# Performance work log

Measured on AMD Instinct MI355X. Metric: run time of the kernel, lower is better.

## Reference

```python
import jax, jax.numpy as jnp
import numpy as np


def _gcn_conv(x, edge_index, W, b):
    """Standard PyG GCNConv: add self-loops, symmetric normalization, x@W, scatter-add, +bias."""
    n = x.shape[0]
    loop = jnp.arange(n, dtype=edge_index.dtype)
    src = jnp.concatenate([edge_index[0], loop])  # [E+N]
    dst = jnp.concatenate([edge_index[1], loop])  # [E+N]
    # degree of destination nodes (unit edge weights + self loops)
    deg = jax.ops.segment_sum(jnp.ones_like(dst, dtype=x.dtype), dst, num_segments=n)
    dinv = jnp.where(deg > 0, jax.lax.rsqrt(deg), 0.0)
    norm = dinv[src] * dinv[dst]  # [E+N]
    h = x @ W  # [N, C_out] -- transform before aggregation (fewer bytes moved)
    msg = h[src] * norm[:, None]  # gather + scale
    out = jax.ops.segment_sum(msg, dst, num_segments=n)  # scatter-add
    return out + b


def setup_inputs() -> dict:
    key = jax.random.key(0)
    k1, k2, k3, k4 = jax.random.split(key, 4)
    N, E, C_in, C_hid, C_out = 50000, 800000, 64, 64, 40
    x = jax.random.normal(k1, (N, C_in), dtype=jnp.float32)
    edge_index = jax.random.randint(k2, (2, E), 0, N, dtype=jnp.int64)
    # Glorot-ish init for weights, zeros for biases (PyG GCNConv default)
    W1 = jax.random.normal(k3, (C_in, C_hid), dtype=jnp.float32) * (1.0 / np.sqrt(C_in))
    b1 = jnp.zeros((C_hid,), dtype=jnp.float32)
    W2 = jax.random.normal(k4, (C_hid, C_out), dtype=jnp.float32) * (1.0 / np.sqrt(C_hid))
    b2 = jnp.zeros((C_out,), dtype=jnp.float32)
    return {"x": x, "edge_index": edge_index, "W1": W1, "b1": b1, "W2": W2, "b2": b2}


def reference(x, edge_index, W1, b1, W2, b2):
    h = jax.nn.relu(_gcn_conv(x, edge_index, W1, b1))
    # F.dropout(training=False) is identity in eval mode
    h = _gcn_conv(h, edge_index, W2, b2)
    return jax.nn.log_softmax(h, axis=1)
```

## Files before the change

### kernel.cpp

```cpp
#include <hip/hip_runtime.h>
#include <hip/hip_fp16.h>
#include <math.h>


#define SHIFT   8
#define RPB     256
#define NBMAX   256
#define SLACK   8192
#define CHUNK_P 2048

typedef float v2f __attribute__((ext_vector_type(2)));

__global__ void k_part_gemm(const int* __restrict__ ei32,
                            int* __restrict__ bcur,
                            unsigned int* __restrict__ ebkt, int E, int nb,
                            int npart,
                            const float* __restrict__ x,
                            const float* __restrict__ W1,
                            unsigned char* __restrict__ hs8, int n) {
    __shared__ __align__(16) float smem[2 * 64 * 68];
    if ((int)blockIdx.x < npart) {
        int* cnt   = (int*)smem;
        int* rbase = cnt + 256;
        int* is64p = rbase + 256;
        int* stash = is64p + 1;
        int t = threadIdx.x;
        cnt[t] = 0;
        if (t == 0) {
            int is64 = 1;
            for (int i = 0; i < 64; ++i)
                if (ei32[2 * i + 1] != 0) { is64 = 0; break; }
            *is64p = is64;
        }
        __syncthreads();
        int is64 = *is64p;
        int lo = blockIdx.x * CHUNK_P;
        int hi = lo + CHUNK_P; if (hi > E) hi = E;
        for (int e = lo + t; e < hi; e += 256) {
            int s, d;
            if (is64) { s = ei32[2 * e]; d = ei32[2 * (E + e)]; }
            else      { s = ei32[e];     d = ei32[E + e]; }
            stash[e - lo] = (int)(((unsigned int)d << 16) | (unsigned int)s);
            atomicAdd(&cnt[d >> SHIFT], 1);
        }
        __syncthreads();
        {
            int c = cnt[t];
            rbase[t] = c ? atomicAdd(&bcur[t], c) : 0;
            cnt[t] = 0;
        }
        __syncthreads();
        for (int e = lo + t; e < hi; e += 256) {
            unsigned int v = (unsigned int)stash[e - lo];
            int b = (int)(v >> 16) >> SHIFT;
            int pos = rbase[b] + atomicAdd(&cnt[b], 1);
            ebkt[pos] = (((v >> 16) & (RPB - 1)) << 16) | (v & 0xffffu);
        }
    } else {
        float* Wl = smem;
        float* Xl = smem + 64 * 68;
        int t  = threadIdx.x;
        int tr = t >> 4, tc = t & 15;
        int base = (blockIdx.x - npart) * 64;

        for (int i = t; i < 64 * 17; i += 256) {
            int k = i / 17, c4 = (i % 17) * 4;
            float4 w = make_float4(0.f, 0.f, 0.f, 0.f);
            if (c4 < 64) w = *(const float4*)&W1[k * 64 + c4];
            *(float4*)&Wl[k * 68 + c4] = w;
        }
        for (int rr = tr; rr < 64; rr += 16) {
            int row = base + rr; if (row >= n) row = n - 1;
            float4 v = *(const float4*)&x[(size_t)row * 64 + tc * 4];
            Xl[(tc * 4 + 0) * 68 + rr] = v.x;
            Xl[(tc * 4 + 1) * 68 + rr] = v.y;
            Xl[(tc * 4 + 2) * 68 + rr] = v.z;
            Xl[(tc * 4 + 3) * 68 + rr] = v.w;
        }
        __syncthreads();

        float acc[4][4] = {{0.f}};
#pragma unroll 8
        for (int k = 0; k < 64; ++k) {
            float4 xv = *(const float4*)&Xl[k * 68 + tr * 4];
            float4 wv = *(const float4*)&Wl[k * 68 + tc * 4];
            acc[0][0] = fmaf(xv.x, wv.x, acc[0][0]);
            acc[0][1] = fmaf(xv.x, wv.y, acc[0][1]);
            acc[0][2] = fmaf(xv.x, wv.z, acc[0][2]);
            acc[0][3] = fmaf(xv.x, wv.w, acc[0][3]);
            acc[1][0] = fmaf(xv.y, wv.x, acc[1][0]);
            acc[1][1] = fmaf(xv.y, wv.y, acc[1][1]);
            acc[1][2] = fmaf(xv.y, wv.z, acc[1][2]);
            acc[1][3] = fmaf(xv.y, wv.w, acc[1][3]);
            acc[2][0] = fmaf(xv.z, wv.x, acc[2][0]);
            acc[2][1] = fmaf(xv.z, wv.y, acc[2][1]);
            acc[2][2] = fmaf(xv.z, wv.z, acc[2][2]);
            acc[2][3] = fmaf(xv.z, wv.w, acc[2][3]);
            acc[3][0] = fmaf(xv.w, wv.x, acc[3][0]);
            acc[3][1] = fmaf(xv.w, wv.y, acc[3][1]);
            acc[3][2] = fmaf(xv.w, wv.z, acc[3][2]);
            acc[3][3] = fmaf(xv.w, wv.w, acc[3][3]);
        }
#pragma unroll
        for (int i = 0; i < 4; ++i) {
            int r = base + tr * 4 + i;
            if (r >= n) break;
            unsigned int w;
            w = (unsigned int)__builtin_amdgcn_cvt_pk_fp8_f32(
                    acc[i][0], acc[i][1], 0, false);
            w = (unsigned int)__builtin_amdgcn_cvt_pk_fp8_f32(
                    acc[i][2], acc[i][3], (int)w, true);
            ((unsigned int*)(hs8 + ((size_t)r << 6)))[tc] = w;
        }
    }
}

__global__ void k_build(const unsigned int* __restrict__ ebkt,
                        const int* __restrict__ bcur,
                        int* __restrict__ row_beg, int* __restrict__ row_end,
                        float* __restrict__ dinv,
                        unsigned short* __restrict__ csr_src, int N) {
    __shared__ int cnt[RPB];
    __shared__ int ssum[RPB];
    int t = threadIdx.x, b = blockIdx.x;
    int rows0 = b << SHIFT;
    cnt[t] = 0;
    __syncthreads();
    int lo = b * SLACK, hi = bcur[b];
    for (int e = lo + t; e < hi; e += 256)
        atomicAdd(&cnt[ebkt[e] >> 16], 1);
    __syncthreads();
    int c = cnt[t];
    ssum[t] = c;
    __syncthreads();
    for (int off = 1; off < 256; off <<= 1) {
        int u = (t >= off) ? ssum[t - off] : 0;
        __syncthreads();
        ssum[t] += u;
        __syncthreads();
    }
    int beg = lo + ssum[t] - c;
    int row = rows0 + t;
    if (row < N) {
        row_beg[row] = beg; row_end[row] = beg + c;
        dinv[row] = rsqrtf((float)c + 1.0f);
    }
    cnt[t] = beg;
    __syncthreads();
    for (int e = lo + t; e < hi; e += 256) {
        unsigned int v = ebkt[e];
        int pos = atomicAdd(&cnt[v >> 16], 1);
        csr_src[pos] = (unsigned short)(v & 0xffffu);
    }
}

__global__ void k_gather_relu64(const unsigned char* __restrict__ hs8,
                                const int* __restrict__ rbg,
                                const int* __restrict__ ren,
                                const unsigned short* __restrict__ ci,
                                const float* __restrict__ dinv,
                                const float* __restrict__ bias,
                                __half* __restrict__ out, int n) {
    int row = blockIdx.x * 4 + (threadIdx.x >> 6);
    if (row >= n) return;
    int lane = threadIdx.x & 63;
    int g = lane >> 3, q = lane & 7;
    int beg = rbg[row], end = ren[row];

    float dv = dinv[row];
    uint2 su = ((const uint2*)(hs8 + ((size_t)row << 6)))[q];

    float4 aa = make_float4(0.f, 0.f, 0.f, 0.f);
    float4 ab = make_float4(0.f, 0.f, 0.f, 0.f);
    for (int base = beg; base < end; base += 64) {
        int mm = end - base; if (mm > 64) mm = 64;
        int idx = (lane < mm) ? (int)ci[base + lane] : 0;
        for (int j = 0; 8 * j < mm; ++j) {
            int e = 8 * j + g;
            int s = __shfl(idx, e, 64);
            if (base + e < end) {
                float ds = dinv[s];
                uint2 u = ((const uint2*)(hs8 + ((size_t)s << 6)))[q];
                v2f f0 = __builtin_amdgcn_cvt_pk_f32_fp8((int)u.x, false);
                v2f f1 = __builtin_amdgcn_cvt_pk_f32_fp8((int)u.x, true);
                v2f f2 = __builtin_amdgcn_cvt_pk_f32_fp8((int)u.y, false);
                v2f f3 = __builtin_amdgcn_cvt_pk_f32_fp8((int)u.y, true);
                aa.x = fmaf(f0.x, ds, aa.x); aa.y = fmaf(f0.y, ds, aa.y);
                aa.z = fmaf(f1.x, ds, aa.z); aa.w = fmaf(f1.y, ds, aa.w);
                ab.x = fmaf(f2.x, ds, ab.x); ab.y = fmaf(f2.y, ds, ab.y);
                ab.z = fmaf(f3.x, ds, ab.z); ab.w = fmaf(f3.y, ds, ab.w);
            }
        }
    }
#pragma unroll
    for (int o = 8; o < 64; o <<= 1) {
        aa.x += __shfl_xor(aa.x, o, 64); aa.y += __shfl_xor(aa.y, o, 64);
        aa.z += __shfl_xor(aa.z, o, 64); aa.w += __shfl_xor(aa.w, o, 64);
        ab.x += __shfl_xor(ab.x, o, 64); ab.y += __shfl_xor(ab.y, o, 64);
        ab.z += __shfl_xor(ab.z, o, 64); ab.w += __shfl_xor(ab.w, o, 64);
    }
    v2f s0 = __builtin_amdgcn_cvt_pk_f32_fp8((int)su.x, false);
    v2f s1 = __builtin_amdgcn_cvt_pk_f32_fp8((int)su.x, true);
    v2f s2 = __builtin_amdgcn_cvt_pk_f32_fp8((int)su.y, false);
    v2f s3 = __builtin_amdgcn_cvt_pk_f32_fp8((int)su.y, true);
    float4 bv0 = *(const float4*)&bias[q * 8];
    float4 bv1 = *(const float4*)&bias[q * 8 + 4];
    float v0 = fmaxf((aa.x + s0.x * dv) * dv + bv0.x, 0.f);
    float v1 = fmaxf((aa.y + s0.y * dv) * dv + bv0.y, 0.f);
    float v2 = fmaxf((aa.z + s1.x * dv) * dv + bv0.z, 0.f);
    float v3 = fmaxf((aa.w + s1.y * dv) * dv + bv0.w, 0.f);
    float v4 = fmaxf((ab.x + s2.x * dv) * dv + bv1.x, 0.f);
    float v5 = fmaxf((ab.y + s2.y * dv) * dv + bv1.y, 0.f);
    float v6 = fmaxf((ab.z + s3.x * dv) * dv + bv1.z, 0.f);
    float v7 = fmaxf((ab.w + s3.y * dv) * dv + bv1.w, 0.f);
    if (lane < 8) {
        uint4 st;
        ((__half2*)&st)[0] = __floats2half2_rn(v0, v1);
        ((__half2*)&st)[1] = __floats2half2_rn(v2, v3);
        ((__half2*)&st)[2] = __floats2half2_rn(v4, v5);
        ((__half2*)&st)[3] = __floats2half2_rn(v6, v7);
        ((uint4*)(out + ((size_t)row << 6)))[q] = st;
    }
}

template<int COUT>
__global__ void k_gemm(const __half* __restrict__ xin,
                       const float* __restrict__ W,
                       const float* __restrict__ dinv,
                       __half* __restrict__ hs, int n) {
    __shared__ float Wl[64 * 68];
    __shared__ float Xl[64 * 68];
    int t  = threadIdx.x;
    int tr = t >> 4, tc = t & 15;
    int base = blockIdx.x * 64;

    for (int i = t; i < 64 * 17; i += 256) {
        int k = i / 17, c4 = (i % 17) * 4;
        float4 w = make_float4(0.f, 0.f, 0.f, 0.f);
        if (c4 < COUT) w = *(const float4*)&W[k * COUT + c4];
        *(float4*)&Wl[k * 68 + c4] = w;
    }
    for (int rr = tr; rr < 64; rr += 16) {
        int row = base + rr; if (row >= n) row = n - 1;
        uint2 u = *(const uint2*)&xin[(size_t)row * 64 + tc * 4];
        float2 a = __half22float2(*(__half2*)&u.x);
        float2 c = __half22float2(*(__half2*)&u.y);
        Xl[(tc * 4 + 0) * 68 + rr] = a.x;
        Xl[(tc * 4 + 1) * 68 + rr] = a.y;
        Xl[(tc * 4 + 2) * 68 + rr] = c.x;
        Xl[(tc * 4 + 3) * 68 + rr] = c.y;
    }
    __syncthreads();

    float acc[4][4] = {{0.f}};
#pragma unroll 8
    for (int k = 0; k < 64; ++k) {
        float4 xv = *(const float4*)&Xl[k * 68 + tr * 4];
        float4 wv = *(const float4*)&Wl[k * 68 + tc * 4];
        acc[0][0] = fmaf(xv.x, wv.x, acc[0][0]);
        acc[0][1] = fmaf(xv.x, wv.y, acc[0][1]);
        acc[0][2] = fmaf(xv.x, wv.z, acc[0][2]);
        acc[0][3] = fmaf(xv.x, wv.w, acc[0][3]);
        acc[1][0] = fmaf(xv.y, wv.x, acc[1][0]);
        acc[1][1] = fmaf(xv.y, wv.y, acc[1][1]);
        acc[1][2] = fmaf(xv.y, wv.z, acc[1][2]);
        acc[1][3] = fmaf(xv.y, wv.w, acc[1][3]);
        acc[2][0] = fmaf(xv.z, wv.x, acc[2][0]);
        acc[2][1] = fmaf(xv.z, wv.y, acc[2][1]);
        acc[2][2] = fmaf(xv.z, wv.z, acc[2][2]);
        acc[2][3] = fmaf(xv.z, wv.w, acc[2][3]);
        acc[3][0] = fmaf(xv.w, wv.x, acc[3][0]);
        acc[3][1] = fmaf(xv.w, wv.y, acc[3][1]);
        acc[3][2] = fmaf(xv.w, wv.z, acc[3][2]);
        acc[3][3] = fmaf(xv.w, wv.w, acc[3][3]);
    }
#pragma unroll
    for (int i = 0; i < 4; ++i) {
        int r = base + tr * 4 + i;
        if (r >= n) break;
        float dv = dinv[r];
        __half2 p0 = __floats2half2_rn(acc[i][0] * dv, acc[i][1] * dv);
        __half2 p1 = __floats2half2_rn(acc[i][2] * dv, acc[i][3] * dv);
        if (tc * 4 + 3 < COUT) {
            *(__half2*)&hs[(size_t)r * COUT + tc * 4]     = p0;
            *(__half2*)&hs[(size_t)r * COUT + tc * 4 + 2] = p1;
        }
    }
}

__global__ void k_gather_lsm40(const __half* __restrict__ hs,
                               const int* __restrict__ rbg,
                               const int* __restrict__ ren,
                               const unsigned short* __restrict__ ci,
                               const float* __restrict__ dinv,
                               const float* __restrict__ bias,
                               float* __restrict__ out, int n) {
    int row = blockIdx.x * 4 + (threadIdx.x >> 6);
    if (row >= n) return;
    int lane = threadIdx.x & 63;
    int g = lane >> 4, q = lane & 15;
    int beg = rbg[row], end = ren[row];

    float dv = dinv[row];
    uint2 selfu = make_uint2(0u, 0u);
    if (q < 10)
        selfu = ((const uint2*)(hs + (size_t)row * 40))[q];

    float4 a = make_float4(0.f, 0.f, 0.f, 0.f);
    for (int base = beg; base < end; base += 64) {
        int mm = end - base; if (mm > 64) mm = 64;
        int idx = (lane < mm) ? (int)ci[base + lane] : 0;
        for (int j = 0; 4 * j < mm; ++j) {
            int s = __shfl(idx, 4 * j + g, 64);
            if (q < 10 && base + 4 * j + g < end) {
                uint2 u = ((const uint2*)(hs + (size_t)s * 40))[q];
                float2 f0 = __half22float2(*(__half2*)&u.x);
                float2 f1 = __half22float2(*(__half2*)&u.y);
                a.x += f0.x; a.y += f0.y; a.z += f1.x; a.w += f1.y;
            }
        }
    }
    a.x += __shfl_xor(a.x, 16, 64); a.y += __shfl_xor(a.y, 16, 64);
    a.z += __shfl_xor(a.z, 16, 64); a.w += __shfl_xor(a.w, 16, 64);
    a.x += __shfl_xor(a.x, 32, 64); a.y += __shfl_xor(a.y, 32, 64);
    a.z += __shfl_xor(a.z, 32, 64); a.w += __shfl_xor(a.w, 32, 64);

    float2 s0 = __half22float2(*(__half2*)&selfu.x);
    float2 s1 = __half22float2(*(__half2*)&selfu.y);
    float v0 = -INFINITY, v1 = -INFINITY, v2 = -INFINITY, v3 = -INFINITY;
    if (q < 10) {
        float4 bv = *(const float4*)&bias[q * 4];
        v0 = (a.x + s0.x) * dv + bv.x;
        v1 = (a.y + s0.y) * dv + bv.y;
        v2 = (a.z + s1.x) * dv + bv.z;
        v3 = (a.w + s1.y) * dv + bv.w;
    }
    float mx = fmaxf(fmaxf(v0, v1), fmaxf(v2, v3));
#pragma unroll
    for (int o = 1; o < 16; o <<= 1) mx = fmaxf(mx, __shfl_xor(mx, o, 64));
    float e0 = (q < 10) ? expf(v0 - mx) : 0.f;
    float e1 = (q < 10) ? expf(v1 - mx) : 0.f;
    float e2 = (q < 10) ? expf(v2 - mx) : 0.f;
    float e3 = (q < 10) ? expf(v3 - mx) : 0.f;
    float sm = (e0 + e1) + (e2 + e3);
#pragma unroll
    for (int o = 1; o < 16; o <<= 1) sm += __shfl_xor(sm, o, 64);
    if (lane < 16 && q < 10) {
        float ls = logf(sm);
        float4 r = make_float4(v0 - mx - ls, v1 - mx - ls,
                               v2 - mx - ls, v3 - mx - ls);
        *(float4*)&out[(size_t)row * 40 + q * 4] = r;
    }
}

extern "C" void kernel_launch(void* const* d_in, const int* in_sizes, int n_in,
                              void* d_out, int out_size, void* d_ws, size_t ws_size,
                              hipStream_t stream) {
    const float* x  = (const float*)d_in[0];
    const void*  ei = d_in[1];
    const float* W1 = (const float*)d_in[2];
    const float* b1 = (const float*)d_in[3];
    const float* W2 = (const float*)d_in[4];
    const float* b2 = (const float*)d_in[5];
    float* out = (float*)d_out;

    const int C_IN = 64;
    const int N = in_sizes[0] / C_IN;
    const int E = in_sizes[1] / 2;
    (void)n_in; (void)out_size; (void)ws_size;

    char* ws = (char*)d_ws;
    size_t off = 0;
    auto alloc = [&](size_t bytes) -> void* {
        void* p = ws + off;
        off += (bytes + 255) & ~(size_t)255;
        return p;
    };
    int*            bcur    = (int*)           alloc(NBMAX * 4);
    unsigned int*   ebkt    = (unsigned int*)  alloc((size_t)NBMAX * SLACK * 4);
    unsigned short* csr_src = (unsigned short*)alloc((size_t)NBMAX * SLACK * 2);
    int*            row_beg = (int*)           alloc((size_t)N * 4);
    int*            row_end = (int*)           alloc((size_t)N * 4);
    float*          dinv    = (float*)         alloc((size_t)N * 4);
    unsigned char*  hs8     = (unsigned char*) alloc((size_t)N * 64);
    __half*         h1b     = (__half*)        alloc((size_t)N * 64 * 2);
    __half*         hs2     = (__half*)        alloc((size_t)N * 40 * 2);

    const int nb    = (N + RPB - 1) >> SHIFT;
    const int ngrid = (N + 63) / 64;
    const int npart = (E + CHUNK_P - 1) / CHUNK_P;

    static int h_binit[NBMAX];
    for (int i = 0; i < NBMAX; ++i) h_binit[i] = i * SLACK;
    (void)hipMemcpyAsync(bcur, h_binit, NBMAX * sizeof(int),
                         hipMemcpyHostToDevice, stream);

    k_part_gemm<<<npart + ngrid, 256, 0, stream>>>(
        (const int*)ei, bcur, ebkt, E, nb, npart, x, W1, hs8, N);
    k_build<<<nb, 256, 0, stream>>>(ebkt, bcur, row_beg, row_end, dinv,
                                    csr_src, N);
    k_gather_relu64<<<(N + 3) / 4, 256, 0, stream>>>(
        hs8, row_beg, row_end, csr_src, dinv, b1, h1b, N);
    k_gemm<40><<<ngrid, 256, 0, stream>>>(h1b, W2, dinv, hs2, N);
    k_gather_lsm40<<<(N + 3) / 4, 256, 0, stream>>>(
        hs2, row_beg, row_end, csr_src, dinv, b2, out, N);
}
```

Baseline: 105.7 us.

## Pre-scale layer-1 features by source dinv in build kernel, drop per-edge dinv gather

```diff
diff --git a/kernel.cpp b/kernel.cpp
--- a/kernel.cpp
+++ b/kernel.cpp
@@ -17,7 +17,7 @@
                             int npart,
                             const float* __restrict__ x,
                             const float* __restrict__ W1,
-                            unsigned char* __restrict__ hs8, int n) {
+                            __half* __restrict__ hs16, int n) {
     __shared__ __align__(16) float smem[2 * 64 * 68];
     if ((int)blockIdx.x < npart) {
         int* cnt   = (int*)smem;
@@ -105,12 +105,10 @@
         for (int i = 0; i < 4; ++i) {
             int r = base + tr * 4 + i;
             if (r >= n) break;
-            unsigned int w;
-            w = (unsigned int)__builtin_amdgcn_cvt_pk_fp8_f32(
-                    acc[i][0], acc[i][1], 0, false);
-            w = (unsigned int)__builtin_amdgcn_cvt_pk_fp8_f32(
-                    acc[i][2], acc[i][3], (int)w, true);
-            ((unsigned int*)(hs8 + ((size_t)r << 6)))[tc] = w;
+            __half2 p0 = __floats2half2_rn(acc[i][0], acc[i][1]);
+            __half2 p1 = __floats2half2_rn(acc[i][2], acc[i][3]);
+            *(__half2*)&hs16[(size_t)r * 64 + tc * 4]     = p0;
+            *(__half2*)&hs16[(size_t)r * 64 + tc * 4 + 2] = p1;
         }
     }
 }
@@ -119,11 +117,15 @@
                         const int* __restrict__ bcur,
                         int* __restrict__ row_beg, int* __restrict__ row_end,
                         float* __restrict__ dinv,
-                        unsigned short* __restrict__ csr_src, int N) {
+                        unsigned short* __restrict__ csr_src,
+                        const __half* __restrict__ hs16,
+                        unsigned char* __restrict__ hs8, int N) {
     __shared__ int cnt[RPB];
     __shared__ int ssum[RPB];
+    __shared__ float dinv_l[RPB];
     int t = threadIdx.x, b = blockIdx.x;
     int rows0 = b << SHIFT;
+    int nrows = N - rows0; if (nrows > RPB) nrows = RPB;
     cnt[t] = 0;
     __syncthreads();
     int lo = b * SLACK, hi = bcur[b];
@@ -140,10 +142,12 @@
         __syncthreads();
     }
     int beg = lo + ssum[t] - c;
+    float dvt = rsqrtf((float)c + 1.0f);
+    dinv_l[t] = dvt;
     int row = rows0 + t;
     if (row < N) {
         row_beg[row] = beg; row_end[row] = beg + c;
-        dinv[row] = rsqrtf((float)c + 1.0f);
+        dinv[row] = dvt;
     }
     cnt[t] = beg;
     __syncthreads();
@@ -151,6 +155,26 @@
         unsigned int v = ebkt[e];
         int pos = atomicAdd(&cnt[v >> 16], 1);
         csr_src[pos] = (unsigned short)(v & 0xffffu);
+    }
+    for (int i = t; i < nrows * 8; i += 256) {
+        int r = i >> 3, piece = i & 7;
+        float dv = dinv_l[r];
+        uint4 u = ((const uint4*)(hs16 + ((size_t)(rows0 + r) << 6)))[piece];
+        float2 f0 = __half22float2(*(__half2*)&u.x);
+        float2 f1 = __half22float2(*(__half2*)&u.y);
+        float2 f2 = __half22float2(*(__half2*)&u.z);
+        float2 f3 = __half22float2(*(__half2*)&u.w);
+        unsigned int w0, w1;
+        w0 = (unsigned int)__builtin_amdgcn_cvt_pk_fp8_f32(
+                f0.x * dv, f0.y * dv, 0, false);
+        w0 = (unsigned int)__builtin_amdgcn_cvt_pk_fp8_f32(
+                f1.x * dv, f1.y * dv, (int)w0, true);
+        w1 = (unsigned int)__builtin_amdgcn_cvt_pk_fp8_f32(
+                f2.x * dv, f2.y * dv, 0, false);
+        w1 = (unsigned int)__builtin_amdgcn_cvt_pk_fp8_f32(
+                f3.x * dv, f3.y * dv, (int)w1, true);
+        uint2 st; st.x = w0; st.y = w1;
+        ((uint2*)(hs8 + ((size_t)(rows0 + r) << 6)))[piece] = st;
     }
 }
 
@@ -179,16 +203,15 @@
             int e = 8 * j + g;
             int s = __shfl(idx, e, 64);
             if (base + e < end) {
-                float ds = dinv[s];
                 uint2 u = ((const uint2*)(hs8 + ((size_t)s << 6)))[q];
                 v2f f0 = __builtin_amdgcn_cvt_pk_f32_fp8((int)u.x, false);
                 v2f f1 = __builtin_amdgcn_cvt_pk_f32_fp8((int)u.x, true);
                 v2f f2 = __builtin_amdgcn_cvt_pk_f32_fp8((int)u.y, false);
                 v2f f3 = __builtin_amdgcn_cvt_pk_f32_fp8((int)u.y, true);
-                aa.x = fmaf(f0.x, ds, aa.x); aa.y = fmaf(f0.y, ds, aa.y);
-                aa.z = fmaf(f1.x, ds, aa.z); aa.w = fmaf(f1.y, ds, aa.w);
-                ab.x = fmaf(f2.x, ds, ab.x); ab.y = fmaf(f2.y, ds, ab.y);
-                ab.z = fmaf(f3.x, ds, ab.z); ab.w = fmaf(f3.y, ds, ab.w);
+                aa.x += f0.x; aa.y += f0.y;
+                aa.z += f1.x; aa.w += f1.y;
+                ab.x += f2.x; ab.y += f2.y;
+                ab.z += f3.x; ab.w += f3.y;
             }
         }
     }
@@ -205,14 +228,14 @@
     v2f s3 = __builtin_amdgcn_cvt_pk_f32_fp8((int)su.y, true);
     float4 bv0 = *(const float4*)&bias[q * 8];
     float4 bv1 = *(const float4*)&bias[q * 8 + 4];
-    float v0 = fmaxf((aa.x + s0.x * dv) * dv + bv0.x, 0.f);
-    float v1 = fmaxf((aa.y + s0.y * dv) * dv + bv0.y, 0.f);
-    float v2 = fmaxf((aa.z + s1.x * dv) * dv + bv0.z, 0.f);
-    float v3 = fmaxf((aa.w + s1.y * dv) * dv + bv0.w, 0.f);
-    float v4 = fmaxf((ab.x + s2.x * dv) * dv + bv1.x, 0.f);
-    float v5 = fmaxf((ab.y + s2.y * dv) * dv + bv1.y, 0.f);
-    float v6 = fmaxf((ab.z + s3.x * dv) * dv + bv1.z, 0.f);
-    float v7 = fmaxf((ab.w + s3.y * dv) * dv + bv1.w, 0.f);
+    float v0 = fmaxf((aa.x + s0.x) * dv + bv0.x, 0.f);
+    float v1 = fmaxf((aa.y + s0.y) * dv + bv0.y, 0.f);
+    float v2 = fmaxf((aa.z + s1.x) * dv + bv0.z, 0.f);
+    float v3 = fmaxf((aa.w + s1.y) * dv + bv0.w, 0.f);
+    float v4 = fmaxf((ab.x + s2.x) * dv + bv1.x, 0.f);
+    float v5 = fmaxf((ab.y + s2.y) * dv + bv1.y, 0.f);
+    float v6 = fmaxf((ab.z + s3.x) * dv + bv1.z, 0.f);
+    float v7 = fmaxf((ab.w + s3.y) * dv + bv1.w, 0.f);
     if (lane < 8) {
         uint4 st;
         ((__half2*)&st)[0] = __floats2half2_rn(v0, v1);
@@ -382,6 +405,7 @@
     int*            row_beg = (int*)           alloc((size_t)N * 4);
     int*            row_end = (int*)           alloc((size_t)N * 4);
     float*          dinv    = (float*)         alloc((size_t)N * 4);
+    __half*         hs16    = (__half*)        alloc((size_t)N * 64 * 2);
     unsigned char*  hs8     = (unsigned char*) alloc((size_t)N * 64);
     __half*         h1b     = (__half*)        alloc((size_t)N * 64 * 2);
     __half*         hs2     = (__half*)        alloc((size_t)N * 40 * 2);
@@ -396,9 +420,9 @@
                          hipMemcpyHostToDevice, stream);
 
     k_part_gemm<<<npart + ngrid, 256, 0, stream>>>(
-        (const int*)ei, bcur, ebkt, E, nb, npart, x, W1, hs8, N);
+        (const int*)ei, bcur, ebkt, E, nb, npart, x, W1, hs16, N);
     k_build<<<nb, 256, 0, stream>>>(ebkt, bcur, row_beg, row_end, dinv,
-                                    csr_src, N);
+                                    csr_src, hs16, hs8, N);
     k_gather_relu64<<<(N + 3) / 4, 256, 0, stream>>>(
         hs8, row_beg, row_end, csr_src, dinv, b1, h1b, N);
     k_gemm<40><<<ngrid, 256, 0, stream>>>(h1b, W2, dinv, hs2, N);
```

After: 109.0 us. +3.1%, slower.
